# Optimization experiments

Hardware: AMD Instinct MI355X
Metric: run time of the kernel (lower is better)

## Reference

```python
import jax, jax.numpy as jnp
import numpy as np

WS = 4        # window_size
HEADS = 4     # num_heads
DIM = 128

def _rel_pos_idx(ws):
    # (ws*ws, ws*ws) int index into (2*ws-1)^2 bias table, as in Swin
    coords = np.stack(np.meshgrid(np.arange(ws), np.arange(ws), indexing='ij'))  # (2,ws,ws)
    cf = coords.reshape(2, -1)                       # (2, n)
    rel = cf[:, :, None] - cf[:, None, :]            # (2, n, n)
    rel = rel.transpose(1, 2, 0).astype(np.int64)    # (n, n, 2)
    rel[:, :, 0] += ws - 1
    rel[:, :, 1] += ws - 1
    rel[:, :, 0] *= 2 * ws - 1
    return jnp.asarray(rel.sum(-1))                  # (n, n)

def setup_inputs() -> dict:
    key = jax.random.key(0)
    ks = jax.random.split(key, 6)
    B, H, W, C = 16, 128, 128, DIM
    return {
        "x": jax.random.normal(ks[0], (B, H * W, C), dtype=jnp.float32),
        "H": H,
        "W": W,
        "qkv_w": jax.random.normal(ks[1], (C, 3 * C), dtype=jnp.float32) * 0.02,
        "qkv_b": jax.random.normal(ks[2], (3 * C,), dtype=jnp.float32) * 0.02,
        "proj_w": jax.random.normal(ks[3], (C, C), dtype=jnp.float32) * 0.02,
        "proj_b": jax.random.normal(ks[4], (C,), dtype=jnp.float32) * 0.02,
        "bias_tbl": jax.random.normal(ks[5], ((2 * WS - 1) ** 2, HEADS), dtype=jnp.float32) * 0.02,
    }

def reference(x, H, W, qkv_w, qkv_b, proj_w, proj_b, bias_tbl):
    B, N, C = x.shape
    hd = C // HEADS
    scale = hd ** -0.5
    n = WS * WS
    Hn, Wn = H // WS, W // WS
    # window partition: (B,N,C) -> (B*nW, ws*ws, C)
    xw = x.reshape(B, Hn, WS, Wn, WS, C).transpose(0, 1, 3, 2, 4, 5).reshape(-1, n, C)
    nW = xw.shape[0]
    qkv = xw @ qkv_w + qkv_b                               # (nW, n, 3C)
    qkv = qkv.reshape(nW, n, 3, HEADS, hd).transpose(2, 0, 3, 1, 4)
    q, k, v = qkv[0], qkv[1], qkv[2]                       # (nW, heads, n, hd)
    attn = jnp.einsum('whnd,whmd->whnm', q, k) * scale     # (nW, heads, n, n)
    idx = _rel_pos_idx(WS)
    bias = bias_tbl[idx.reshape(-1)].reshape(n, n, HEADS).transpose(2, 0, 1)  # (heads,n,n)
    attn = jax.nn.softmax(attn + bias[None], axis=-1)
    out = jnp.einsum('whnm,whmd->whnd', attn, v)           # (nW, heads, n, hd)
    out = out.transpose(0, 2, 1, 3).reshape(nW, n, C)
    out = out @ proj_w + proj_b
    # window reverse: (B*nW, n, C) -> (B, N, C)
    out = out.reshape(B, Hn, Wn, WS, WS, C).transpose(0, 1, 3, 2, 4, 5).reshape(B, N, C)
    return out
```

## Files before the change

### kernel.cpp

```cpp
#include <hip/hip_runtime.h>

typedef unsigned short u16;
typedef unsigned int   u32;
typedef __attribute__((ext_vector_type(8))) short bf16x8;
typedef __attribute__((ext_vector_type(4))) short bf16x4;
typedef __attribute__((ext_vector_type(4))) float f32x4;
typedef __attribute__((ext_vector_type(2))) u32 u32x2;

union F8 { bf16x8 v; u32 u[4]; };
union F4 { bf16x4 v; u32 u[2]; };

__device__ __forceinline__ u16 f2b(float f) {
    unsigned u = __builtin_bit_cast(unsigned, f);
    return (u16)((u + 0x7FFFu + ((u >> 16) & 1u)) >> 16);
}
__device__ __forceinline__ u32 rneu(u32 u) { return u + 0x7FFFu + ((u >> 16) & 1u); }
__device__ __forceinline__ u32 pkbf(float a, float b) {
#if __has_builtin(__builtin_amdgcn_perm)
    u32 ua = rneu(__builtin_bit_cast(u32, a));
    u32 ub = rneu(__builtin_bit_cast(u32, b));
    return __builtin_amdgcn_perm(ub, ua, 0x07060302u);
#else
    return ((u32)f2b(b) << 16) | (u32)f2b(a);
#endif
}

__device__ __forceinline__ f32x4 mfma16(F4 a, F4 b, f32x4 c) {
    F8 a8, b8;
    a8.u[0] = a.u[0]; a8.u[1] = a.u[1]; a8.u[2] = 0; a8.u[3] = 0;
    b8.u[0] = b.u[0]; b8.u[1] = b.u[1]; b8.u[2] = 0; b8.u[3] = 0;
    return __builtin_amdgcn_mfma_f32_16x16x32_bf16(a8.v, b8.v, c, 0, 0, 0);
}

__device__ __forceinline__ void stage_tile(const u16* wfrag, u16* ldsbase,
                                           int t, int wave, int lane) {
    const char* gp = (const char*)wfrag + (((t * 4 + wave) << 10) | (lane << 4));
    char* lp = (char*)ldsbase + (((t % 3) << 12) | (wave << 10));
    __builtin_amdgcn_global_load_lds(
        (const __attribute__((address_space(1))) void*)gp,
        (__attribute__((address_space(3))) void*)lp, 16, 0, 0);
}

#define PIPE_WAIT(N) { asm volatile("s_waitcnt vmcnt(" #N ")" ::: "memory"); \
    __builtin_amdgcn_sched_barrier(0); __builtin_amdgcn_s_barrier(); }

__global__ void prep_kernel(const float* __restrict__ qkv_w,
                            const float* __restrict__ proj_w,
                            const float* __restrict__ bias_tbl,
                            const float* __restrict__ qkv_b,
                            u16* __restrict__ wsb, float* __restrict__ wsf)
{
    const float scale = 0.17677669529663689f;
    int tid = blockIdx.x * 256 + threadIdx.x;
    if (tid < 49152) {
        int i = tid & 7, l = (tid >> 3) & 63, w = (tid >> 9) & 3, t = tid >> 11;
        int nt;
        if (t < 16) { int h = t >> 2, r = t & 3;
                      nt = (r < 2) ? (2 * h + r) : (8 + 2 * h + (r - 2)); }
        else nt = t;
        int k = w * 32 + (l >> 4) * 8 + i;
        int col = nt * 16 + (l & 15);
        float wv = qkv_w[k * 384 + col];
        if (col < 128) wv *= scale;
        wsb[tid] = f2b(wv);
    } else if (tid < 57344) {
        int e = tid - 49152;
        int nt = e >> 10, rem = e & 1023;
        int c = rem >> 7, le = rem & 127, l = le >> 1, j = le & 1;
        int col = nt * 16 + (l & 15);
        int d = c * 16 + 4 * (l >> 4) + 2 * j;
        u32 val = ((u32)f2b(proj_w[(d + 1) * 128 + col]) << 16)
                |  (u32)f2b(proj_w[d * 128 + col]);
        ((u32*)wsb)[(24 + nt) * 1024 + c * 128 + l * 2 + j] = val;
    } else if (tid < 58368) {
        int e = tid - 57344;
        int h = e >> 8, t1 = (e >> 4) & 15, t2 = e & 15;
        int idx = ((t1 >> 2) - (t2 >> 2) + 3) * 7 + ((t1 & 3) - (t2 & 3) + 3);
        wsf[32768 + e] = bias_tbl[idx * 4 + h];
    } else if (tid < 58752) {
        int e = tid - 58368;
        wsf[33792 + e] = qkv_b[e] * (e < 128 ? scale : 1.0f);
    }
}

__global__ __launch_bounds__(256, 4) void winattn_kernel(
    const float* __restrict__ x, const u16* __restrict__ wfrag,
    const float* __restrict__ proj_b, float* __restrict__ out)
{
    __shared__ alignas(16) u16 lds[9216];
    u16* ring = lds;
    float* qkvbL  = (float*)(lds + 6144);
    float* biasL  = (float*)(lds + 6912);
    float* projbL = (float*)(lds + 8960);

    const int tid  = threadIdx.x;
    const int wave = tid >> 6, lane = tid & 63;
    const int g = lane >> 4, q16 = lane & 15;

    const float* wsf = (const float*)wfrag;
    for (int e = tid; e < 384;  e += 256) qkvbL[e] = wsf[33792 + e];
    for (int e = tid; e < 1024; e += 256) biasL[e] = wsf[32768 + e];
    if (tid < 128) projbL[tid] = proj_b[tid];

    const int wpair = blockIdx.x * 4 + wave;
    const int wid0  = wpair * 2;
    const int b = wid0 >> 10, rem = wid0 & 1023, wi = rem >> 5, wj = rem & 31;
    const int nTok = (wi * 4 + (q16 >> 2)) * 128 + wj * 4 + (q16 & 3);
    const float* xrowA = x + ((long)b * 16384 + nTok) * 128;
    const float* xrowB = xrowA + 512;

    F8 axA[4], axB[4];
    #pragma unroll
    for (int ks = 0; ks < 4; ++ks) {
        const float4* pA = (const float4*)(xrowA + ks * 32 + g * 8);
        float4 a0 = pA[0], a1 = pA[1];
        axA[ks].u[0] = pkbf(a0.x, a0.y); axA[ks].u[1] = pkbf(a0.z, a0.w);
        axA[ks].u[2] = pkbf(a1.x, a1.y); axA[ks].u[3] = pkbf(a1.z, a1.w);
        const float4* pB = (const float4*)(xrowB + ks * 32 + g * 8);
        float4 b0 = pB[0], b1 = pB[1];
        axB[ks].u[0] = pkbf(b0.x, b0.y); axB[ks].u[1] = pkbf(b0.z, b0.w);
        axB[ks].u[2] = pkbf(b1.x, b1.y); axB[ks].u[3] = pkbf(b1.z, b1.w);
    }
    __builtin_amdgcn_sched_barrier(0);
    __syncthreads();

    stage_tile(wfrag, lds, 0, wave, lane);
    stage_tile(wfrag, lds, 1, wave, lane);

    f32x4 z4 = {0.f, 0.f, 0.f, 0.f};
    F4 ones; ones.u[0] = 0x3f803f80u; ones.u[1] = 0x3f803f80u;
    F4 pPA[4], pPB[4];
    float rsA4[4], rsB4[4];
    u32 OpkA[8][2], OpkB[8][2];

    #define QKV_TILE(T, NT, P0A, P1A, P0B, P1B) {                              \
        const u16* slot = ring + ((T) % 3) * 2048;                             \
        float4 bb = *(const float4*)&qkvbL[(NT) * 16 + 4 * g];                 \
        f32x4 accA = {bb.x, bb.y, bb.z, bb.w}, accB = accA;                    \
        _Pragma("unroll")                                                      \
        for (int ks = 0; ks < 4; ++ks) {                                       \
            bf16x8 frag = *(const bf16x8*)(slot + ks * 512 + lane * 8);        \
            accA = __builtin_amdgcn_mfma_f32_16x16x32_bf16(frag, axA[ks].v, accA, 0, 0, 0); \
            accB = __builtin_amdgcn_mfma_f32_16x16x32_bf16(frag, axB[ks].v, accB, 0, 0, 0); \
        }                                                                      \
        P0A = pkbf(accA[0], accA[1]); P1A = pkbf(accA[2], accA[3]);            \
        P0B = pkbf(accB[0], accB[1]); P1B = pkbf(accB[2], accB[3]);            \
    }

    #pragma unroll
    for (int h = 0; h < 4; ++h) {
        u32 QA[2][2], QB[2][2], KA[2][2], KB[2][2];
        #pragma unroll
        for (int r = 0; r < 4; ++r) {
            int t = 4 * h + r;
            PIPE_WAIT(1);
            int nt = (r < 2) ? (2 * h + r) : (8 + 2 * h + (r - 2));
            if (r == 0)      QKV_TILE(t, nt, QA[0][0], QA[0][1], QB[0][0], QB[0][1])
            else if (r == 1) QKV_TILE(t, nt, QA[1][0], QA[1][1], QB[1][0], QB[1][1])
            else if (r == 2) QKV_TILE(t, nt, KA[0][0], KA[0][1], KB[0][0], KB[0][1])
            else             QKV_TILE(t, nt, KA[1][0], KA[1][1], KB[1][0], KB[1][1])
            stage_tile(wfrag, lds, t + 2, wave, lane);
        }
        F8 kfA, qfA, kfB, qfB;
        kfA.u[0]=KA[0][0]; kfA.u[1]=KA[0][1]; kfA.u[2]=KA[1][0]; kfA.u[3]=KA[1][1];
        qfA.u[0]=QA[0][0]; qfA.u[1]=QA[0][1]; qfA.u[2]=QA[1][0]; qfA.u[3]=QA[1][1];
        kfB.u[0]=KB[0][0]; kfB.u[1]=KB[0][1]; kfB.u[2]=KB[1][0]; kfB.u[3]=KB[1][1];
        qfB.u[0]=QB[0][0]; qfB.u[1]=QB[0][1]; qfB.u[2]=QB[1][0]; qfB.u[3]=QB[1][1];
        f32x4 sA = __builtin_amdgcn_mfma_f32_16x16x32_bf16(kfA.v, qfA.v, z4, 0, 0, 0);
        f32x4 sB = __builtin_amdgcn_mfma_f32_16x16x32_bf16(kfB.v, qfB.v, z4, 0, 0, 0);
        float4 bias4 = *(const float4*)&biasL[(h * 16 + q16) * 16 + 4 * g];
        float eA0 = __expf(sA[0] + bias4.x), eA1 = __expf(sA[1] + bias4.y);
        float eA2 = __expf(sA[2] + bias4.z), eA3 = __expf(sA[3] + bias4.w);
        float eB0 = __expf(sB[0] + bias4.x), eB1 = __expf(sB[1] + bias4.y);
        float eB2 = __expf(sB[2] + bias4.z), eB3 = __expf(sB[3] + bias4.w);
        pPA[h].u[0] = pkbf(eA0, eA1); pPA[h].u[1] = pkbf(eA2, eA3);
        pPB[h].u[0] = pkbf(eB0, eB1); pPB[h].u[1] = pkbf(eB2, eB3);
        f32x4 suA = mfma16(ones, pPA[h], z4);
        f32x4 suB = mfma16(ones, pPB[h], z4);
        rsA4[h] = 1.0f / suA[0];
        rsB4[h] = 1.0f / suB[0];
    }

    #pragma unroll
    for (int c = 0; c < 8; ++c) {
        int t = 16 + c;
        PIPE_WAIT(1);
        const u16* slot = ring + (t % 3) * 2048;
        float bvA = qkvbL[(16 + c) * 16 + q16];
        f32x4 accA = {bvA, bvA, bvA, bvA}, accB = accA;
        #pragma unroll
        for (int ks = 0; ks < 4; ++ks) {
            bf16x8 frag = *(const bf16x8*)(slot + ks * 512 + lane * 8);
            accA = __builtin_amdgcn_mfma_f32_16x16x32_bf16(axA[ks].v, frag, accA, 0, 0, 0);
            accB = __builtin_amdgcn_mfma_f32_16x16x32_bf16(axB[ks].v, frag, accB, 0, 0, 0);
        }
        F4 vpA; vpA.u[0] = pkbf(accA[0], accA[1]); vpA.u[1] = pkbf(accA[2], accA[3]);
        F4 vpB; vpB.u[0] = pkbf(accB[0], accB[1]); vpB.u[1] = pkbf(accB[2], accB[3]);
        int hh = c >> 1;
        f32x4 oA = mfma16(vpA, pPA[hh], z4);
        f32x4 oB = mfma16(vpB, pPB[hh], z4);
        float ra = rsA4[hh], rb = rsB4[hh];
        OpkA[c][0] = pkbf(oA[0] * ra, oA[1] * ra);
        OpkA[c][1] = pkbf(oA[2] * ra, oA[3] * ra);
        OpkB[c][0] = pkbf(oB[0] * rb, oB[1] * rb);
        OpkB[c][1] = pkbf(oB[2] * rb, oB[3] * rb);
        stage_tile(wfrag, lds, t + 2, wave, lane);
    }

    const long obaseA = ((long)b * 16384 + nTok) * 128;
    const long obaseB = obaseA + 512;
    #pragma unroll
    for (int nt = 0; nt < 8; ++nt) {
        int t = 24 + nt;
        if (nt == 0)      PIPE_WAIT(1)
        else if (nt == 7) PIPE_WAIT(2)
        else              PIPE_WAIT(3)
        const u32* slot32 = (const u32*)(ring + (t % 3) * 2048);
        float4 pb = *(const float4*)&projbL[nt * 16 + 4 * g];
        f32x4 accA = {pb.x, pb.y, pb.z, pb.w}, accB = accA;
        #pragma unroll
        for (int cp = 0; cp < 4; ++cp) {
            int c = 2 * cp;
            u32x2 wa = *(const u32x2*)&slot32[c * 128 + lane * 2];
            u32x2 wb = *(const u32x2*)&slot32[(c + 1) * 128 + lane * 2];
            F8 wf; wf.u[0] = wa.x; wf.u[1] = wa.y; wf.u[2] = wb.x; wf.u[3] = wb.y;
            F8 bA; bA.u[0] = OpkA[c][0]; bA.u[1] = OpkA[c][1];
                   bA.u[2] = OpkA[c+1][0]; bA.u[3] = OpkA[c+1][1];
            F8 bB; bB.u[0] = OpkB[c][0]; bB.u[1] = OpkB[c][1];
                   bB.u[2] = OpkB[c+1][0]; bB.u[3] = OpkB[c+1][1];
            accA = __builtin_amdgcn_mfma_f32_16x16x32_bf16(wf.v, bA.v, accA, 0, 0, 0);
            accB = __builtin_amdgcn_mfma_f32_16x16x32_bf16(wf.v, bB.v, accB, 0, 0, 0);
        }
        float4 oA; oA.x = accA[0]; oA.y = accA[1]; oA.z = accA[2]; oA.w = accA[3];
        *(float4*)&out[obaseA + nt * 16 + 4 * g] = oA;
        float4 oB; oB.x = accB[0]; oB.y = accB[1]; oB.z = accB[2]; oB.w = accB[3];
        *(float4*)&out[obaseB + nt * 16 + 4 * g] = oB;
        if (nt < 6) stage_tile(wfrag, lds, t + 2, wave, lane);
    }
}

extern "C" void kernel_launch(void* const* d_in, const int* in_sizes, int n_in,
                              void* d_out, int out_size, void* d_ws, size_t ws_size,
                              hipStream_t stream)
{
    const float* x        = (const float*)d_in[0];
    const float* qkv_w    = (const float*)d_in[3];
    const float* qkv_b    = (const float*)d_in[4];
    const float* proj_w   = (const float*)d_in[5];
    const float* proj_b   = (const float*)d_in[6];
    const float* bias_tbl = (const float*)d_in[7];

    u16*   wsb = (u16*)d_ws;
    float* wsf = (float*)d_ws;

    prep_kernel<<<230, 256, 0, stream>>>(qkv_w, proj_w, bias_tbl, qkv_b, wsb, wsf);
    winattn_kernel<<<2048, 256, 0, stream>>>(x, wsb, proj_b, (float*)d_out);
}
```

Before: 73.05 us.

## Use 512-thread blocks and stage weight tiles in pairs to halve barriers

Each block grows from 4 to 8 waves, and the weight-tile ring now holds pairs of 16-column tiles, so each wait-plus-barrier covers two tiles of MFMA work instead of one. This halves the number of pipeline barriers and spreads each weight tile's LDS staging across more waves, with half as many blocks launched. In exchange, LDS per block rises to about 30 KB and barriers now synchronize 8 waves, which can add skew, and the launch bounds change may affect register allocation and occupancy.

```diff
diff --git a/kernel.cpp b/kernel.cpp
--- a/kernel.cpp
+++ b/kernel.cpp
@@ -32,10 +32,10 @@
     return __builtin_amdgcn_mfma_f32_16x16x32_bf16(a8.v, b8.v, c, 0, 0, 0);
 }
 
-__device__ __forceinline__ void stage_tile(const u16* wfrag, u16* ldsbase,
-                                           int t, int wave, int lane) {
-    const char* gp = (const char*)wfrag + (((t * 4 + wave) << 10) | (lane << 4));
-    char* lp = (char*)ldsbase + (((t % 3) << 12) | (wave << 10));
+__device__ __forceinline__ void stage_pair(const u16* wfrag, u16* ldsbase,
+                                           int p, int wave, int lane) {
+    const char* gp = (const char*)wfrag + (((p * 8 + wave) << 10) | (lane << 4));
+    char* lp = (char*)ldsbase + (((p % 3) << 13) | (wave << 10));
     __builtin_amdgcn_global_load_lds(
         (const __attribute__((address_space(1))) void*)gp,
         (__attribute__((address_space(3))) void*)lp, 16, 0, 0);
@@ -83,26 +83,26 @@
     }
 }
 
-__global__ __launch_bounds__(256, 4) void winattn_kernel(
+__global__ __launch_bounds__(512, 6) void winattn_kernel(
     const float* __restrict__ x, const u16* __restrict__ wfrag,
     const float* __restrict__ proj_b, float* __restrict__ out)
 {
-    __shared__ alignas(16) u16 lds[9216];
+    __shared__ alignas(16) u16 lds[15360];
     u16* ring = lds;
-    float* qkvbL  = (float*)(lds + 6144);
-    float* biasL  = (float*)(lds + 6912);
-    float* projbL = (float*)(lds + 8960);
+    float* qkvbL  = (float*)(lds + 12288);
+    float* biasL  = (float*)(lds + 13056);
+    float* projbL = (float*)(lds + 15104);
 
     const int tid  = threadIdx.x;
     const int wave = tid >> 6, lane = tid & 63;
     const int g = lane >> 4, q16 = lane & 15;
 
     const float* wsf = (const float*)wfrag;
-    for (int e = tid; e < 384;  e += 256) qkvbL[e] = wsf[33792 + e];
-    for (int e = tid; e < 1024; e += 256) biasL[e] = wsf[32768 + e];
+    for (int e = tid; e < 384;  e += 512) qkvbL[e] = wsf[33792 + e];
+    for (int e = tid; e < 1024; e += 512) biasL[e] = wsf[32768 + e];
     if (tid < 128) projbL[tid] = proj_b[tid];
 
-    const int wpair = blockIdx.x * 4 + wave;
+    const int wpair = blockIdx.x * 8 + wave;
     const int wid0  = wpair * 2;
     const int b = wid0 >> 10, rem = wid0 & 1023, wi = rem >> 5, wj = rem & 31;
     const int nTok = (wi * 4 + (q16 >> 2)) * 128 + wj * 4 + (q16 & 3);
@@ -124,8 +124,8 @@
     __builtin_amdgcn_sched_barrier(0);
     __syncthreads();
 
-    stage_tile(wfrag, lds, 0, wave, lane);
-    stage_tile(wfrag, lds, 1, wave, lane);
+    stage_pair(wfrag, lds, 0, wave, lane);
+    stage_pair(wfrag, lds, 1, wave, lane);
 
     f32x4 z4 = {0.f, 0.f, 0.f, 0.f};
     F4 ones; ones.u[0] = 0x3f803f80u; ones.u[1] = 0x3f803f80u;
@@ -133,8 +133,8 @@
     float rsA4[4], rsB4[4];
     u32 OpkA[8][2], OpkB[8][2];
 
-    #define QKV_TILE(T, NT, P0A, P1A, P0B, P1B) {                              \
-        const u16* slot = ring + ((T) % 3) * 2048;                             \
+    #define QKV_TILE(P, S, NT, P0A, P1A, P0B, P1B) {                           \
+        const u16* slot = ring + ((P) % 3) * 4096 + (S) * 2048;                \
         float4 bb = *(const float4*)&qkvbL[(NT) * 16 + 4 * g];                 \
         f32x4 accA = {bb.x, bb.y, bb.z, bb.w}, accB = accA;                    \
         _Pragma("unroll")                                                      \
@@ -150,17 +150,14 @@
     #pragma unroll
     for (int h = 0; h < 4; ++h) {
         u32 QA[2][2], QB[2][2], KA[2][2], KB[2][2];
-        #pragma unroll
-        for (int r = 0; r < 4; ++r) {
-            int t = 4 * h + r;
-            PIPE_WAIT(1);
-            int nt = (r < 2) ? (2 * h + r) : (8 + 2 * h + (r - 2));
-            if (r == 0)      QKV_TILE(t, nt, QA[0][0], QA[0][1], QB[0][0], QB[0][1])
-            else if (r == 1) QKV_TILE(t, nt, QA[1][0], QA[1][1], QB[1][0], QB[1][1])
-            else if (r == 2) QKV_TILE(t, nt, KA[0][0], KA[0][1], KB[0][0], KB[0][1])
-            else             QKV_TILE(t, nt, KA[1][0], KA[1][1], KB[1][0], KB[1][1])
-            stage_tile(wfrag, lds, t + 2, wave, lane);
-        }
+        PIPE_WAIT(1);
+        QKV_TILE(2*h, 0, 2*h,     QA[0][0], QA[0][1], QB[0][0], QB[0][1]);
+        QKV_TILE(2*h, 1, 2*h + 1, QA[1][0], QA[1][1], QB[1][0], QB[1][1]);
+        stage_pair(wfrag, lds, 2*h + 2, wave, lane);
+        PIPE_WAIT(1);
+        QKV_TILE(2*h + 1, 0, 8 + 2*h, KA[0][0], KA[0][1], KB[0][0], KB[0][1]);
+        QKV_TILE(2*h + 1, 1, 9 + 2*h, KA[1][0], KA[1][1], KB[1][0], KB[1][1]);
+        stage_pair(wfrag, lds, 2*h + 3, wave, lane);
         F8 kfA, qfA, kfB, qfB;
         kfA.u[0]=KA[0][0]; kfA.u[1]=KA[0][1]; kfA.u[2]=KA[1][0]; kfA.u[3]=KA[1][1];
         qfA.u[0]=QA[0][0]; qfA.u[1]=QA[0][1]; qfA.u[2]=QA[1][0]; qfA.u[3]=QA[1][1];
@@ -182,60 +179,65 @@
     }
 
     #pragma unroll
-    for (int c = 0; c < 8; ++c) {
-        int t = 16 + c;
+    for (int f = 0; f < 4; ++f) {
         PIPE_WAIT(1);
-        const u16* slot = ring + (t % 3) * 2048;
-        float bvA = qkvbL[(16 + c) * 16 + q16];
-        f32x4 accA = {bvA, bvA, bvA, bvA}, accB = accA;
         #pragma unroll
-        for (int ks = 0; ks < 4; ++ks) {
-            bf16x8 frag = *(const bf16x8*)(slot + ks * 512 + lane * 8);
-            accA = __builtin_amdgcn_mfma_f32_16x16x32_bf16(axA[ks].v, frag, accA, 0, 0, 0);
-            accB = __builtin_amdgcn_mfma_f32_16x16x32_bf16(axB[ks].v, frag, accB, 0, 0, 0);
+        for (int s = 0; s < 2; ++s) {
+            int c = 2 * f + s;
+            const u16* slot = ring + ((8 + f) % 3) * 4096 + s * 2048;
+            float bvA = qkvbL[(16 + c) * 16 + q16];
+            f32x4 accA = {bvA, bvA, bvA, bvA}, accB = accA;
+            #pragma unroll
+            for (int ks = 0; ks < 4; ++ks) {
+                bf16x8 frag = *(const bf16x8*)(slot + ks * 512 + lane * 8);
+                accA = __builtin_amdgcn_mfma_f32_16x16x32_bf16(axA[ks].v, frag, accA, 0, 0, 0);
+                accB = __builtin_amdgcn_mfma_f32_16x16x32_bf16(axB[ks].v, frag, accB, 0, 0, 0);
+            }
+            F4 vpA; vpA.u[0] = pkbf(accA[0], accA[1]); vpA.u[1] = pkbf(accA[2], accA[3]);
+            F4 vpB; vpB.u[0] = pkbf(accB[0], accB[1]); vpB.u[1] = pkbf(accB[2], accB[3]);
+            f32x4 oA = mfma16(vpA, pPA[f], z4);
+            f32x4 oB = mfma16(vpB, pPB[f], z4);
+            float ra = rsA4[f], rb = rsB4[f];
+            OpkA[c][0] = pkbf(oA[0] * ra, oA[1] * ra);
+            OpkA[c][1] = pkbf(oA[2] * ra, oA[3] * ra);
+            OpkB[c][0] = pkbf(oB[0] * rb, oB[1] * rb);
+            OpkB[c][1] = pkbf(oB[2] * rb, oB[3] * rb);
         }
-        F4 vpA; vpA.u[0] = pkbf(accA[0], accA[1]); vpA.u[1] = pkbf(accA[2], accA[3]);
-        F4 vpB; vpB.u[0] = pkbf(accB[0], accB[1]); vpB.u[1] = pkbf(accB[2], accB[3]);
-        int hh = c >> 1;
-        f32x4 oA = mfma16(vpA, pPA[hh], z4);
-        f32x4 oB = mfma16(vpB, pPB[hh], z4);
-        float ra = rsA4[hh], rb = rsB4[hh];
-        OpkA[c][0] = pkbf(oA[0] * ra, oA[1] * ra);
-        OpkA[c][1] = pkbf(oA[2] * ra, oA[3] * ra);
-        OpkB[c][0] = pkbf(oB[0] * rb, oB[1] * rb);
-        OpkB[c][1] = pkbf(oB[2] * rb, oB[3] * rb);
-        stage_tile(wfrag, lds, t + 2, wave, lane);
+        stage_pair(wfrag, lds, 10 + f, wave, lane);
     }
 
     const long obaseA = ((long)b * 16384 + nTok) * 128;
     const long obaseB = obaseA + 512;
     #pragma unroll
-    for (int nt = 0; nt < 8; ++nt) {
-        int t = 24 + nt;
-        if (nt == 0)      PIPE_WAIT(1)
-        else if (nt == 7) PIPE_WAIT(2)
-        else              PIPE_WAIT(3)
-        const u32* slot32 = (const u32*)(ring + (t % 3) * 2048);
-        float4 pb = *(const float4*)&projbL[nt * 16 + 4 * g];
-        f32x4 accA = {pb.x, pb.y, pb.z, pb.w}, accB = accA;
+    for (int f = 0; f < 4; ++f) {
+        if (f == 0)      PIPE_WAIT(1)
+        else if (f == 3) PIPE_WAIT(4)
+        else             PIPE_WAIT(5)
         #pragma unroll
-        for (int cp = 0; cp < 4; ++cp) {
-            int c = 2 * cp;
-            u32x2 wa = *(const u32x2*)&slot32[c * 128 + lane * 2];
-            u32x2 wb = *(const u32x2*)&slot32[(c + 1) * 128 + lane * 2];
-            F8 wf; wf.u[0] = wa.x; wf.u[1] = wa.y; wf.u[2] = wb.x; wf.u[3] = wb.y;
-            F8 bA; bA.u[0] = OpkA[c][0]; bA.u[1] = OpkA[c][1];
-                   bA.u[2] = OpkA[c+1][0]; bA.u[3] = OpkA[c+1][1];
-            F8 bB; bB.u[0] = OpkB[c][0]; bB.u[1] = OpkB[c][1];
-                   bB.u[2] = OpkB[c+1][0]; bB.u[3] = OpkB[c+1][1];
-            accA = __builtin_amdgcn_mfma_f32_16x16x32_bf16(wf.v, bA.v, accA, 0, 0, 0);
-            accB = __builtin_amdgcn_mfma_f32_16x16x32_bf16(wf.v, bB.v, accB, 0, 0, 0);
+        for (int s = 0; s < 2; ++s) {
+            int nt = 2 * f + s;
+            const u32* slot32 = (const u32*)(ring + ((12 + f) % 3) * 4096 + s * 2048);
+            float4 pb = *(const float4*)&projbL[nt * 16 + 4 * g];
+            f32x4 accA = {pb.x, pb.y, pb.z, pb.w}, accB = accA;
+            #pragma unroll
+            for (int cp = 0; cp < 4; ++cp) {
+                int c = 2 * cp;
+                u32x2 wa = *(const u32x2*)&slot32[c * 128 + lane * 2];
+                u32x2 wb = *(const u32x2*)&slot32[(c + 1) * 128 + lane * 2];
+                F8 wf; wf.u[0] = wa.x; wf.u[1] = wa.y; wf.u[2] = wb.x; wf.u[3] = wb.y;
+                F8 bA; bA.u[0] = OpkA[c][0]; bA.u[1] = OpkA[c][1];
+                       bA.u[2] = OpkA[c+1][0]; bA.u[3] = OpkA[c+1][1];
+                F8 bB; bB.u[0] = OpkB[c][0]; bB.u[1] = OpkB[c][1];
+                       bB.u[2] = OpkB[c+1][0]; bB.u[3] = OpkB[c+1][1];
+                accA = __builtin_amdgcn_mfma_f32_16x16x32_bf16(wf.v, bA.v, accA, 0, 0, 0);
+                accB = __builtin_amdgcn_mfma_f32_16x16x32_bf16(wf.v, bB.v, accB, 0, 0, 0);
+            }
+            float4 oA; oA.x = accA[0]; oA.y = accA[1]; oA.z = accA[2]; oA.w = accA[3];
+            *(float4*)&out[obaseA + nt * 16 + 4 * g] = oA;
+            float4 oB; oB.x = accB[0]; oB.y = accB[1]; oB.z = accB[2]; oB.w = accB[3];
+            *(float4*)&out[obaseB + nt * 16 + 4 * g] = oB;
         }
-        float4 oA; oA.x = accA[0]; oA.y = accA[1]; oA.z = accA[2]; oA.w = accA[3];
-        *(float4*)&out[obaseA + nt * 16 + 4 * g] = oA;
-        float4 oB; oB.x = accB[0]; oB.y = accB[1]; oB.z = accB[2]; oB.w = accB[3];
-        *(float4*)&out[obaseB + nt * 16 + 4 * g] = oB;
-        if (nt < 6) stage_tile(wfrag, lds, t + 2, wave, lane);
+        if (f < 2) stage_pair(wfrag, lds, 14 + f, wave, lane);
     }
 }
 
@@ -254,5 +256,5 @@
     float* wsf = (float*)d_ws;
 
     prep_kernel<<<230, 256, 0, stream>>>(qkv_w, proj_w, bias_tbl, qkv_b, wsb, wsf);
-    winattn_kernel<<<2048, 256, 0, stream>>>(x, wsb, proj_b, (float*)d_out);
-}
+    winattn_kernel<<<1024, 512, 0, stream>>>(x, wsb, proj_b, (float*)d_out);
+}
```

Result: slower. 174.8 us (+139.3%).
